# Optimization experiments

Hardware: AMD Instinct MI355X
Metric: run time of the kernel (lower is better)

The kernel has to match this reference:

```python
import jax, jax.numpy as jnp
import numpy as np
from jax import lax


def setup_inputs() -> dict:
    key = jax.random.key(0)
    k1, k2 = jax.random.split(key)
    B, H, W, C = 8, 32, 32, 512
    N = 16384
    feature_batch = jax.random.normal(k1, (B, H, W, C), dtype=jnp.float32)
    mb = jax.random.normal(k2, (N, C), dtype=jnp.float32)
    return {"feature_batch": feature_batch, "mb": mb, "b": 9}


def reference(feature_batch, mb, b):
    B, H, W, C = feature_batch.shape
    fv = feature_batch.reshape(B * H * W, C)                       # (Q, C)
    sq = (
        jnp.sum(fv * fv, axis=1)[:, None]
        + jnp.sum(mb * mb, axis=1)[None, :]
        - 2.0 * (fv @ mb.T)
    )                                                               # (Q, N)
    sq = jnp.maximum(sq, 0.0)  # guard fp round-off before sqrt
    # smallest-b distances, sorted ascending (top_k of negated values)
    neg_topk = lax.top_k(-sq, b)[0]                                 # (Q, b)
    top_k_dists_squared = -neg_topk
    pixel_scores = jnp.sqrt(top_k_dists_squared[:, 0]).reshape(B, H * W)
    max_idx = jnp.argmax(pixel_scores, axis=1)                      # (B,)
    softmax_args = jnp.sqrt(
        top_k_dists_squared.reshape(B, H * W, b)[jnp.arange(B), max_idx, :]
    )                                                               # (B, b)
    image_scores = softmax_args[:, 0]
    if b > 1:
        image_scores = image_scores * (1.0 - jax.nn.softmax(softmax_args, axis=1)[:, 0])
    pixel_scores = pixel_scores.reshape(B, 1, H, W)
    return pixel_scores, image_scores
```

## Files before the change

kernel.cpp:

```cpp
#include <hip/hip_runtime.h>
#include <hip/hip_bf16.h>

typedef unsigned short u16;

#define M_ROWS 8192
#define N_ROWS 16384
#define KDIM   512
#define BM     128
#define BN     128
#define BK     64
#define NCHUNKS 8
#define NPER   (N_ROWS / NCHUNKS)
#define NT_CNT (NPER / BN)
#define TOPK   9

typedef __attribute__((ext_vector_type(8)))  short bf16x8;
typedef __attribute__((ext_vector_type(16))) float f32x16;

__device__ __forceinline__ void gload_lds16(const void* g, void* l) {
  __builtin_amdgcn_global_load_lds(
      (const __attribute__((address_space(1))) void*)g,
      (__attribute__((address_space(3))) void*)l,
      16, 0, 0);
}

__device__ __forceinline__ u16 f2bf(float x) {
  union { float f; unsigned u; } c; c.f = x;
  unsigned u = c.u;
  u += 0x7fffu + ((u >> 16) & 1u);
  return (u16)(u >> 16);
}

__device__ __forceinline__ void topk_update(float v, float best[TOPK]) {
  if (v < best[TOPK - 1]) {
    #pragma unroll
    for (int i = 0; i < TOPK; ++i) {
      float b = best[i];
      best[i] = fminf(b, v);
      v = fmaxf(b, v);
    }
  }
}

__global__ __launch_bounds__(256) void prep_kernel(
    const float* __restrict__ fv, const float* __restrict__ mb,
    u16* __restrict__ fvb, u16* __restrict__ mbb,
    float* __restrict__ nf, float* __restrict__ nm_perm)
{
  int idx = blockIdx.x * 4 + (threadIdx.x >> 6);
  int l = threadIdx.x & 63;
  const float* src; u16* dst;
  if (idx < M_ROWS) {
    src = fv + (size_t)idx * KDIM; dst = fvb + (size_t)idx * KDIM;
  } else {
    int r = idx - M_ROWS;
    src = mb + (size_t)r * KDIM; dst = mbb + (size_t)r * KDIM;
  }
  float4 x0 = ((const float4*)src)[2 * l];
  float4 x1 = ((const float4*)src)[2 * l + 1];
  float s = x0.x * x0.x + x0.y * x0.y + x0.z * x0.z + x0.w * x0.w
          + x1.x * x1.x + x1.y * x1.y + x1.z * x1.z + x1.w * x1.w;
  uint4 o;
  o.x = (unsigned)f2bf(x0.x) | ((unsigned)f2bf(x0.y) << 16);
  o.y = (unsigned)f2bf(x0.z) | ((unsigned)f2bf(x0.w) << 16);
  o.z = (unsigned)f2bf(x1.x) | ((unsigned)f2bf(x1.y) << 16);
  o.w = (unsigned)f2bf(x1.z) | ((unsigned)f2bf(x1.w) << 16);
  ((uint4*)dst)[l] = o;
  #pragma unroll
  for (int off = 32; off > 0; off >>= 1) s += __shfl_down(s, off, 64);
  if (l == 0) {
    if (idx < M_ROWS) {
      nf[idx] = s;
    } else {
      int n  = idx - M_ROWS;
      int ig = n >> 5;
      int w5 = n & 31;
      int h  = (w5 >> 2) & 1;
      int r  = (w5 & 3) | ((w5 >> 3) << 2);
      nm_perm[(ig * 2 + h) * 16 + r] = s;
    }
  }
}

__global__ __launch_bounds__(256) void gemm_topk_kernel(
    const u16* __restrict__ fvb, const u16* __restrict__ mbb,
    const float* __restrict__ nm_perm, float* __restrict__ partial)
{
  __shared__ __align__(16) u16 As[2][BM * BK];
  __shared__ __align__(16) u16 Bs[2][BN * BK];

  const int t   = threadIdx.x;
  const int l   = t & 63;
  const int w   = t >> 6;
  const int wm  = w & 1;
  const int wn  = w >> 1;
  const int h   = l >> 5;
  const int c31 = l & 31;
  const int cx  = c31 & 7;

  const int m0    = blockIdx.x * BM;
  const int ncoff = blockIdx.y * NPER;

  const int srow_lo = l >> 3;
  const int sc      = ((l & 7) ^ srow_lo) * 8;

  float best[2][TOPK];
  float T[2];
  #pragma unroll
  for (int j = 0; j < 2; ++j) {
    T[j] = 3.4e38f;
    #pragma unroll
    for (int i = 0; i < TOPK; ++i) best[j][i] = 3.4e38f;
  }

  {
    const int kb = sc;
    #pragma unroll
    for (int i = 0; i < 4; ++i) {
      gload_lds16(fvb + (size_t)(m0 + w * 32 + i * 8 + srow_lo) * KDIM + kb,
                  &As[0][(w * 32 + i * 8) * BK]);
      gload_lds16(mbb + (size_t)(ncoff + w * 32 + i * 8 + srow_lo) * KDIM + kb,
                  &Bs[0][(w * 32 + i * 8) * BK]);
    }
  }

  for (int nt = 0; nt < NT_CNT; ++nt) {
    const int nbase = ncoff + nt * BN;
    f32x16 acc[2][2];
    #pragma unroll
    for (int i = 0; i < 2; ++i)
      #pragma unroll
      for (int j = 0; j < 2; ++j)
        #pragma unroll
        for (int r = 0; r < 16; ++r) acc[i][j][r] = 0.0f;

    for (int kc = 0; kc < KDIM / BK; ++kc) {
      const int cur = kc & 1;
      __syncthreads();
      if (kc < KDIM / BK - 1) {
        const int kb = (kc + 1) * BK + sc;
        #pragma unroll
        for (int i = 0; i < 4; ++i) {
          gload_lds16(fvb + (size_t)(m0 + w * 32 + i * 8 + srow_lo) * KDIM + kb,
                      &As[cur ^ 1][(w * 32 + i * 8) * BK]);
          gload_lds16(mbb + (size_t)(nbase + w * 32 + i * 8 + srow_lo) * KDIM + kb,
                      &Bs[cur ^ 1][(w * 32 + i * 8) * BK]);
        }
      } else if (nt + 1 < NT_CNT) {
        const int kb = sc;
        #pragma unroll
        for (int i = 0; i < 4; ++i) {
          gload_lds16(fvb + (size_t)(m0 + w * 32 + i * 8 + srow_lo) * KDIM + kb,
                      &As[cur ^ 1][(w * 32 + i * 8) * BK]);
          gload_lds16(mbb + (size_t)(nbase + BN + w * 32 + i * 8 + srow_lo) * KDIM + kb,
                      &Bs[cur ^ 1][(w * 32 + i * 8) * BK]);
        }
      }
      #pragma unroll
      for (int kk = 0; kk < 4; ++kk) {
        const int ch = ((kk * 2 + h) ^ cx) * 8;
        bf16x8 fvf0 = *(const bf16x8*)&As[cur][(wm * 64 + c31) * BK + ch];
        bf16x8 fvf1 = *(const bf16x8*)&As[cur][(wm * 64 + 32 + c31) * BK + ch];
        bf16x8 mbf0 = *(const bf16x8*)&Bs[cur][(wn * 64 + c31) * BK + ch];
        bf16x8 mbf1 = *(const bf16x8*)&Bs[cur][(wn * 64 + 32 + c31) * BK + ch];
        acc[0][0] = __builtin_amdgcn_mfma_f32_32x32x16_bf16(mbf0, fvf0, acc[0][0], 0, 0, 0);
        acc[0][1] = __builtin_amdgcn_mfma_f32_32x32x16_bf16(mbf0, fvf1, acc[0][1], 0, 0, 0);
        acc[1][0] = __builtin_amdgcn_mfma_f32_32x32x16_bf16(mbf1, fvf0, acc[1][0], 0, 0, 0);
        acc[1][1] = __builtin_amdgcn_mfma_f32_32x32x16_bf16(mbf1, fvf1, acc[1][1], 0, 0, 0);
      }
    }

    #pragma unroll
    for (int j = 0; j < 2; ++j) {
      float v[32];
      float bmin = 3.4e38f;
      #pragma unroll
      for (int i = 0; i < 2; ++i) {
        const float4* np =
            (const float4*)&nm_perm[((((nbase >> 5) + wn * 2 + i)) * 2 + h) * 16];
        #pragma unroll
        for (int rr = 0; rr < 4; ++rr) {
          float4 q = np[rr];
          v[i * 16 + rr * 4 + 0] = fmaf(-2.0f, acc[i][j][rr * 4 + 0], q.x);
          v[i * 16 + rr * 4 + 1] = fmaf(-2.0f, acc[i][j][rr * 4 + 1], q.y);
          v[i * 16 + rr * 4 + 2] = fmaf(-2.0f, acc[i][j][rr * 4 + 2], q.z);
          v[i * 16 + rr * 4 + 3] = fmaf(-2.0f, acc[i][j][rr * 4 + 3], q.w);
        }
      }
      #pragma unroll
      for (int r = 0; r < 32; ++r) bmin = fminf(bmin, v[r]);
      if (bmin < T[j]) {
        #pragma unroll
        for (int r = 0; r < 32; ++r) topk_update(v[r], best[j]);
      }
      float th = best[j][TOPK - 1];
      T[j] = fminf(th, __shfl_xor(th, 32, 64));
    }
  }

  #pragma unroll
  for (int j = 0; j < 2; ++j) {
    float tmp[TOPK];
    #pragma unroll
    for (int s = 0; s < TOPK; ++s) tmp[s] = __shfl_xor(best[j][s], 32, 64);
    #pragma unroll
    for (int s = 0; s < TOPK; ++s) topk_update(tmp[s], best[j]);
  }
  #pragma unroll
  for (int j = 0; j < 2; ++j) {
    int m = m0 + wm * 64 + j * 32 + c31;
    size_t base = ((size_t)(blockIdx.y * 2 + wn) * M_ROWS + m) * TOPK;
    if (h == 0) {
      #pragma unroll
      for (int s = 0; s < 5; ++s) partial[base + s] = best[j][s];
    } else {
      #pragma unroll
      for (int s = 5; s < TOPK; ++s) partial[base + s] = best[j][s];
    }
  }
}

__global__ __launch_bounds__(256) void merge_kernel(
    const float* __restrict__ partial, const float* __restrict__ nf,
    float* __restrict__ final9, float* __restrict__ out_pix)
{
  int row = blockIdx.x * 256 + threadIdx.x;
  float best[TOPK];
  #pragma unroll
  for (int i = 0; i < TOPK; ++i) best[i] = 3.4e38f;
  for (int s = 0; s < 2 * NCHUNKS; ++s) {
    const float* p = &partial[((size_t)s * M_ROWS + row) * TOPK];
    #pragma unroll
    for (int i = 0; i < TOPK; ++i) topk_update(p[i], best);
  }
  float nfr = nf[row];
  float d[TOPK];
  #pragma unroll
  for (int i = 0; i < TOPK; ++i) d[i] = sqrtf(fmaxf(best[i] + nfr, 0.0f));
  out_pix[row] = d[0];
  #pragma unroll
  for (int i = 0; i < TOPK; ++i) final9[(size_t)row * TOPK + i] = d[i];
}

__global__ __launch_bounds__(256) void img_kernel(
    const float* __restrict__ out_pix, const float* __restrict__ final9,
    const int* __restrict__ bptr, float* __restrict__ out_img)
{
  int img = blockIdx.x, t = threadIdx.x;
  float bv = -1.0f; int bi = 0;
  for (int p = t; p < 1024; p += 256) {
    float v = out_pix[img * 1024 + p];
    if (v > bv) { bv = v; bi = p; }
  }
  __shared__ float sv[256];
  __shared__ int   si[256];
  sv[t] = bv; si[t] = bi;
  __syncthreads();
  for (int off = 128; off > 0; off >>= 1) {
    if (t < off) {
      float v2 = sv[t + off]; int i2 = si[t + off];
      if (v2 > sv[t] || (v2 == sv[t] && i2 < si[t])) { sv[t] = v2; si[t] = i2; }
    }
    __syncthreads();
  }
  if (t == 0) {
    int row = img * 1024 + si[0];
    int b = bptr[0];
    float s0 = final9[(size_t)row * TOPK + 0];
    float score = s0;
    if (b > 1) {
      int bb = b < TOPK ? b : TOPK;
      float mx = s0;
      for (int i = 1; i < bb; ++i) mx = fmaxf(mx, final9[(size_t)row * TOPK + i]);
      float den = 0.0f;
      for (int i = 0; i < bb; ++i) den += expf(final9[(size_t)row * TOPK + i] - mx);
      score = s0 * (1.0f - expf(s0 - mx) / den);
    }
    out_img[img] = score;
  }
}

extern "C" void kernel_launch(void* const* d_in, const int* in_sizes, int n_in,
                              void* d_out, int out_size, void* d_ws, size_t ws_size,
                              hipStream_t stream) {
  const float* fv   = (const float*)d_in[0];
  const float* mb   = (const float*)d_in[1];
  const int*   bptr = (const int*)d_in[2];
  float* out = (float*)d_out;

  char* w = (char*)d_ws;
  u16*   fvb     = (u16*)w;
  u16*   mbb     = (u16*)(w + 8388608);
  float* nf      = (float*)(w + 25165824);
  float* nm_perm = (float*)(w + 25198592);
  float* partial = (float*)(w + 25264128);
  float* final9  = (float*)(w + 29982720);

  hipLaunchKernelGGL(prep_kernel, dim3((M_ROWS + N_ROWS) / 4), dim3(256), 0, stream,
                     fv, mb, fvb, mbb, nf, nm_perm);
  hipLaunchKernelGGL(gemm_topk_kernel, dim3(M_ROWS / BM, NCHUNKS), dim3(256), 0, stream,
                     fvb, mbb, nm_perm, partial);
  hipLaunchKernelGGL(merge_kernel, dim3(M_ROWS / 256), dim3(256), 0, stream,
                     partial, nf, final9, out);
  hipLaunchKernelGGL(img_kernel, dim3(8), dim3(256), 0, stream,
                     out, final9, bptr, out + M_ROWS);
}
```

Measured before the change: 317.7 us.

## Halve K tile, double N chunks, raise occupancy, fuse merge and image scoring

Shrinks the K tile from 64 to 32 and adjusts the LDS swizzle and load pattern to match. Doubles the number of N chunks so more blocks are launched, and sets launch bounds to target 3 blocks per CU. The epilogue now recomputes distances instead of keeping a 32-float array live, to cut register pressure. The separate merge and image kernels are combined into one 8-block scoring kernel, which removes the final9 buffer and a launch. In exchange, the merge now runs over twice as many partial lists with only 8 blocks, so that stage may serialize.

Result: slower. 612.2 us (+92.7%).

```diff
diff --git a/kernel.cpp b/kernel.cpp
--- a/kernel.cpp
+++ b/kernel.cpp
@@ -8,10 +8,11 @@
 #define KDIM   512
 #define BM     128
 #define BN     128
-#define BK     64
-#define NCHUNKS 8
+#define BK     32
+#define NCHUNKS 16
 #define NPER   (N_ROWS / NCHUNKS)
 #define NT_CNT (NPER / BN)
+#define KC_CNT (KDIM / BK)
 #define TOPK   9
 
 typedef __attribute__((ext_vector_type(8)))  short bf16x8;
@@ -82,7 +83,7 @@
   }
 }
 
-__global__ __launch_bounds__(256) void gemm_topk_kernel(
+__global__ __launch_bounds__(256, 3) void gemm_topk_kernel(
     const u16* __restrict__ fvb, const u16* __restrict__ mbb,
     const float* __restrict__ nm_perm, float* __restrict__ partial)
 {
@@ -96,13 +97,13 @@
   const int wn  = w >> 1;
   const int h   = l >> 5;
   const int c31 = l & 31;
-  const int cx  = c31 & 7;
+  const int cx  = c31 & 3;
 
   const int m0    = blockIdx.x * BM;
   const int ncoff = blockIdx.y * NPER;
 
-  const int srow_lo = l >> 3;
-  const int sc      = ((l & 7) ^ srow_lo) * 8;
+  const int srow_lo = l >> 2;
+  const int sc      = ((l & 3) ^ (srow_lo & 3)) * 8;
 
   float best[2][TOPK];
   float T[2];
@@ -114,13 +115,12 @@
   }
 
   {
-    const int kb = sc;
-    #pragma unroll
-    for (int i = 0; i < 4; ++i) {
-      gload_lds16(fvb + (size_t)(m0 + w * 32 + i * 8 + srow_lo) * KDIM + kb,
-                  &As[0][(w * 32 + i * 8) * BK]);
-      gload_lds16(mbb + (size_t)(ncoff + w * 32 + i * 8 + srow_lo) * KDIM + kb,
-                  &Bs[0][(w * 32 + i * 8) * BK]);
+    #pragma unroll
+    for (int g = 0; g < 2; ++g) {
+      gload_lds16(fvb + (size_t)(m0 + w * 32 + g * 16 + srow_lo) * KDIM + sc,
+                  &As[0][(w * 32 + g * 16) * BK]);
+      gload_lds16(mbb + (size_t)(ncoff + w * 32 + g * 16 + srow_lo) * KDIM + sc,
+                  &Bs[0][(w * 32 + g * 16) * BK]);
     }
   }
 
@@ -134,30 +134,29 @@
         #pragma unroll
         for (int r = 0; r < 16; ++r) acc[i][j][r] = 0.0f;
 
-    for (int kc = 0; kc < KDIM / BK; ++kc) {
+    for (int kc = 0; kc < KC_CNT; ++kc) {
       const int cur = kc & 1;
       __syncthreads();
-      if (kc < KDIM / BK - 1) {
+      if (kc < KC_CNT - 1) {
         const int kb = (kc + 1) * BK + sc;
         #pragma unroll
-        for (int i = 0; i < 4; ++i) {
-          gload_lds16(fvb + (size_t)(m0 + w * 32 + i * 8 + srow_lo) * KDIM + kb,
-                      &As[cur ^ 1][(w * 32 + i * 8) * BK]);
-          gload_lds16(mbb + (size_t)(nbase + w * 32 + i * 8 + srow_lo) * KDIM + kb,
-                      &Bs[cur ^ 1][(w * 32 + i * 8) * BK]);
+        for (int g = 0; g < 2; ++g) {
+          gload_lds16(fvb + (size_t)(m0 + w * 32 + g * 16 + srow_lo) * KDIM + kb,
+                      &As[cur ^ 1][(w * 32 + g * 16) * BK]);
+          gload_lds16(mbb + (size_t)(nbase + w * 32 + g * 16 + srow_lo) * KDIM + kb,
+                      &Bs[cur ^ 1][(w * 32 + g * 16) * BK]);
         }
       } else if (nt + 1 < NT_CNT) {
-        const int kb = sc;
-        #pragma unroll
-        for (int i = 0; i < 4; ++i) {
-          gload_lds16(fvb + (size_t)(m0 + w * 32 + i * 8 + srow_lo) * KDIM + kb,
-                      &As[cur ^ 1][(w * 32 + i * 8) * BK]);
-          gload_lds16(mbb + (size_t)(nbase + BN + w * 32 + i * 8 + srow_lo) * KDIM + kb,
-                      &Bs[cur ^ 1][(w * 32 + i * 8) * BK]);
+        #pragma unroll
+        for (int g = 0; g < 2; ++g) {
+          gload_lds16(fvb + (size_t)(m0 + w * 32 + g * 16 + srow_lo) * KDIM + sc,
+                      &As[cur ^ 1][(w * 32 + g * 16) * BK]);
+          gload_lds16(mbb + (size_t)(nbase + BN + w * 32 + g * 16 + srow_lo) * KDIM + sc,
+                      &Bs[cur ^ 1][(w * 32 + g * 16) * BK]);
         }
       }
       #pragma unroll
-      for (int kk = 0; kk < 4; ++kk) {
+      for (int kk = 0; kk < 2; ++kk) {
         const int ch = ((kk * 2 + h) ^ cx) * 8;
         bf16x8 fvf0 = *(const bf16x8*)&As[cur][(wm * 64 + c31) * BK + ch];
         bf16x8 fvf1 = *(const bf16x8*)&As[cur][(wm * 64 + 32 + c31) * BK + ch];
@@ -172,26 +171,34 @@
 
     #pragma unroll
     for (int j = 0; j < 2; ++j) {
-      float v[32];
       float bmin = 3.4e38f;
       #pragma unroll
       for (int i = 0; i < 2; ++i) {
         const float4* np =
-            (const float4*)&nm_perm[((((nbase >> 5) + wn * 2 + i)) * 2 + h) * 16];
+            (const float4*)&nm_perm[(((nbase >> 5) + wn * 2 + i) * 2 + h) * 16];
         #pragma unroll
         for (int rr = 0; rr < 4; ++rr) {
           float4 q = np[rr];
-          v[i * 16 + rr * 4 + 0] = fmaf(-2.0f, acc[i][j][rr * 4 + 0], q.x);
-          v[i * 16 + rr * 4 + 1] = fmaf(-2.0f, acc[i][j][rr * 4 + 1], q.y);
-          v[i * 16 + rr * 4 + 2] = fmaf(-2.0f, acc[i][j][rr * 4 + 2], q.z);
-          v[i * 16 + rr * 4 + 3] = fmaf(-2.0f, acc[i][j][rr * 4 + 3], q.w);
+          bmin = fminf(bmin, fmaf(-2.0f, acc[i][j][rr * 4 + 0], q.x));
+          bmin = fminf(bmin, fmaf(-2.0f, acc[i][j][rr * 4 + 1], q.y));
+          bmin = fminf(bmin, fmaf(-2.0f, acc[i][j][rr * 4 + 2], q.z));
+          bmin = fminf(bmin, fmaf(-2.0f, acc[i][j][rr * 4 + 3], q.w));
         }
       }
-      #pragma unroll
-      for (int r = 0; r < 32; ++r) bmin = fminf(bmin, v[r]);
       if (bmin < T[j]) {
         #pragma unroll
-        for (int r = 0; r < 32; ++r) topk_update(v[r], best[j]);
+        for (int i = 0; i < 2; ++i) {
+          const float4* np =
+              (const float4*)&nm_perm[(((nbase >> 5) + wn * 2 + i) * 2 + h) * 16];
+          #pragma unroll
+          for (int rr = 0; rr < 4; ++rr) {
+            float4 q = np[rr];
+            topk_update(fmaf(-2.0f, acc[i][j][rr * 4 + 0], q.x), best[j]);
+            topk_update(fmaf(-2.0f, acc[i][j][rr * 4 + 1], q.y), best[j]);
+            topk_update(fmaf(-2.0f, acc[i][j][rr * 4 + 2], q.z), best[j]);
+            topk_update(fmaf(-2.0f, acc[i][j][rr * 4 + 3], q.w), best[j]);
+          }
+        }
       }
       float th = best[j][TOPK - 1];
       T[j] = fminf(th, __shfl_xor(th, 32, 64));
@@ -220,41 +227,45 @@
   }
 }
 
-__global__ __launch_bounds__(256) void merge_kernel(
+__global__ __launch_bounds__(256) void scoring_kernel(
     const float* __restrict__ partial, const float* __restrict__ nf,
-    float* __restrict__ final9, float* __restrict__ out_pix)
+    const int* __restrict__ bptr, float* __restrict__ out_pix,
+    float* __restrict__ out_img)
 {
-  int row = blockIdx.x * 256 + threadIdx.x;
-  float best[TOPK];
-  #pragma unroll
-  for (int i = 0; i < TOPK; ++i) best[i] = 3.4e38f;
-  for (int s = 0; s < 2 * NCHUNKS; ++s) {
-    const float* p = &partial[((size_t)s * M_ROWS + row) * TOPK];
-    #pragma unroll
-    for (int i = 0; i < TOPK; ++i) topk_update(p[i], best);
-  }
-  float nfr = nf[row];
-  float d[TOPK];
-  #pragma unroll
-  for (int i = 0; i < TOPK; ++i) d[i] = sqrtf(fmaxf(best[i] + nfr, 0.0f));
-  out_pix[row] = d[0];
-  #pragma unroll
-  for (int i = 0; i < TOPK; ++i) final9[(size_t)row * TOPK + i] = d[i];
-}
-
-__global__ __launch_bounds__(256) void img_kernel(
-    const float* __restrict__ out_pix, const float* __restrict__ final9,
-    const int* __restrict__ bptr, float* __restrict__ out_img)
-{
-  int img = blockIdx.x, t = threadIdx.x;
-  float bv = -1.0f; int bi = 0;
-  for (int p = t; p < 1024; p += 256) {
-    float v = out_pix[img * 1024 + p];
-    if (v > bv) { bv = v; bi = p; }
-  }
+  const int img = blockIdx.x, t = threadIdx.x;
+  __shared__ float sd[256][TOPK];
   __shared__ float sv[256];
   __shared__ int   si[256];
+
+  float bv = -1.0f; int bi = 0;
+  float bd[TOPK];
+  #pragma unroll
+  for (int i = 0; i < TOPK; ++i) bd[i] = 0.0f;
+
+  for (int rr = 0; rr < 4; ++rr) {
+    int row = img * 1024 + rr * 256 + t;
+    float best[TOPK];
+    #pragma unroll
+    for (int i = 0; i < TOPK; ++i) best[i] = 3.4e38f;
+    for (int s = 0; s < 2 * NCHUNKS; ++s) {
+      const float* p = &partial[((size_t)s * M_ROWS + row) * TOPK];
+      #pragma unroll
+      for (int i = 0; i < TOPK; ++i) topk_update(p[i], best);
+    }
+    float nfr = nf[row];
+    float d[TOPK];
+    #pragma unroll
+    for (int i = 0; i < TOPK; ++i) d[i] = sqrtf(fmaxf(best[i] + nfr, 0.0f));
+    out_pix[row] = d[0];
+    if (d[0] > bv) {
+      bv = d[0]; bi = row;
+      #pragma unroll
+      for (int i = 0; i < TOPK; ++i) bd[i] = d[i];
+    }
+  }
   sv[t] = bv; si[t] = bi;
+  #pragma unroll
+  for (int i = 0; i < TOPK; ++i) sd[t][i] = bd[i];
   __syncthreads();
   for (int off = 128; off > 0; off >>= 1) {
     if (t < off) {
@@ -264,16 +275,16 @@
     __syncthreads();
   }
   if (t == 0) {
-    int row = img * 1024 + si[0];
+    int wt = si[0] & 255;
     int b = bptr[0];
-    float s0 = final9[(size_t)row * TOPK + 0];
+    float s0 = sd[wt][0];
     float score = s0;
     if (b > 1) {
       int bb = b < TOPK ? b : TOPK;
       float mx = s0;
-      for (int i = 1; i < bb; ++i) mx = fmaxf(mx, final9[(size_t)row * TOPK + i]);
+      for (int i = 1; i < bb; ++i) mx = fmaxf(mx, sd[wt][i]);
       float den = 0.0f;
-      for (int i = 0; i < bb; ++i) den += expf(final9[(size_t)row * TOPK + i] - mx);
+      for (int i = 0; i < bb; ++i) den += expf(sd[wt][i] - mx);
       score = s0 * (1.0f - expf(s0 - mx) / den);
     }
     out_img[img] = score;
@@ -294,14 +305,11 @@
   float* nf      = (float*)(w + 25165824);
   float* nm_perm = (float*)(w + 25198592);
   float* partial = (float*)(w + 25264128);
-  float* final9  = (float*)(w + 29982720);
 
   hipLaunchKernelGGL(prep_kernel, dim3((M_ROWS + N_ROWS) / 4), dim3(256), 0, stream,
                      fv, mb, fvb, mbb, nf, nm_perm);
   hipLaunchKernelGGL(gemm_topk_kernel, dim3(M_ROWS / BM, NCHUNKS), dim3(256), 0, stream,
                      fvb, mbb, nm_perm, partial);
-  hipLaunchKernelGGL(merge_kernel, dim3(M_ROWS / 256), dim3(256), 0, stream,
-                     partial, nf, final9, out);
-  hipLaunchKernelGGL(img_kernel, dim3(8), dim3(256), 0, stream,
-                     out, final9, bptr, out + M_ROWS);
-}
+  hipLaunchKernelGGL(scoring_kernel, dim3(8), dim3(256), 0, stream,
+                     partial, nf, bptr, out, out + M_ROWS);
+}
```
